# Optimization experiments

Measured on AMD Instinct MI355X. Metric: run time of the kernel, lower is better.

The kernel has to match this reference:

```python
import jax, jax.numpy as jnp
import numpy as np

N = 10000
E = 160000


def _lin(key, fi, fo):
    kw, kb = jax.random.split(key)
    W = jax.random.normal(kw, (fi, fo), dtype=jnp.float32) * 0.02
    b = jnp.zeros((fo,), dtype=jnp.float32)
    return W, b


def setup_inputs() -> dict:
    key = jax.random.key(0)
    ks = jax.random.split(key, 20)
    inp = {}
    inp['x'] = jax.random.normal(ks[0], (N, 2048), dtype=jnp.float32)
    src = jax.random.randint(ks[1], (E,), 0, N)
    dst = jax.random.randint(ks[2], (E,), 0, N)
    inp['edge_index'] = jnp.stack([src, dst]).astype(jnp.int64)
    dims = [(2048, 1024), (1024, 2048), (2048, 1024), (1024, 2048)]
    ki = 3
    for li, (fi, fo) in enumerate(dims, start=1):
        for name in ('q', 'k', 'v', 's'):
            W, b = _lin(ks[ki], fi, fo)
            ki += 1
            inp[f'W{li}{name}'] = W
            inp[f'b{li}{name}'] = b
    return inp


def _tconv(x, src, dst, Wq, bq, Wk, bk, Wv, bv, Ws, bs):
    # PyG TransformerConv, heads=1: per-edge attention j->i, softmax over
    # incoming edges of each target node i, plus root (skip) linear.
    q = x @ Wq + bq                      # [N, C]
    k = x @ Wk + bk
    v = x @ Wv + bv
    C = q.shape[-1]
    logits = jnp.sum(q[dst] * k[src], axis=-1) / jnp.sqrt(jnp.float32(C))  # [E]
    m = jax.ops.segment_max(logits, dst, num_segments=N)   # per-node max
    m = jnp.where(jnp.isfinite(m), m, 0.0)                  # isolated nodes
    e = jnp.exp(logits - m[dst])
    s = jax.ops.segment_sum(e, dst, num_segments=N)
    alpha = e / (s[dst] + 1e-16)                            # [E]
    agg = jax.ops.segment_sum(v[src] * alpha[:, None], dst, num_segments=N)
    return agg + x @ Ws + bs


def reference(x, edge_index,
              W1q, b1q, W1k, b1k, W1v, b1v, W1s, b1s,
              W2q, b2q, W2k, b2k, W2v, b2v, W2s, b2s,
              W3q, b3q, W3k, b3k, W3v, b3v, W3s, b3s,
              W4q, b4q, W4k, b4k, W4v, b4v, W4s, b4s):
    src, dst = edge_index[0], edge_index[1]
    h1 = jax.nn.elu(_tconv(x, src, dst, W1q, b1q, W1k, b1k, W1v, b1v, W1s, b1s))
    h2 = _tconv(h1, src, dst, W2q, b2q, W2k, b2k, W2v, b2v, W2s, b2s)
    h3 = jax.nn.elu(_tconv(h2, src, dst, W3q, b3q, W3k, b3k, W3v, b3v, W3s, b3s))
    out = _tconv(h3, src, dst, W4q, b4q, W4k, b4k, W4v, b4v, W4s, b4s)
    return out
```

## Files before the change

kernel.cpp:

```cpp
#include <hip/hip_runtime.h>
#include <cmath>
#include <cstddef>
#include <cstdint>

typedef __attribute__((ext_vector_type(8))) _Float16 half8_t;
typedef __attribute__((ext_vector_type(4))) _Float16 half4_t;
typedef __attribute__((ext_vector_type(2))) _Float16 half2_t;
typedef __attribute__((ext_vector_type(4))) float f32x4;

__device__ __forceinline__ float dot2f16(half2_t a, half2_t b, float c) {
#if __has_builtin(__builtin_amdgcn_fdot2)
  return __builtin_amdgcn_fdot2(a, b, c, false);
#else
  return c + (float)a.x * (float)b.x + (float)a.y * (float)b.y;
#endif
}

__device__ __forceinline__ void gload16(const unsigned short* g,
                                        unsigned short* l) {
  __builtin_amdgcn_global_load_lds(
      (const __attribute__((address_space(1))) unsigned int*)g,
      (__attribute__((address_space(3))) unsigned int*)l, 16, 0, 0);
}

__global__ __launch_bounds__(256) void cast_f16_k(
    const float* __restrict__ in, unsigned short* __restrict__ out, size_t n4) {
  size_t i = (size_t)blockIdx.x * blockDim.x + threadIdx.x;
  if (i >= n4) return;
  float4 v = ((const float4*)in)[i];
  half4_t h;
  h.x = (_Float16)v.x;
  h.y = (_Float16)v.y;
  h.z = (_Float16)v.z;
  h.w = (_Float16)v.w;
  ((half4_t*)out)[i] = h;
}

__global__ __launch_bounds__(256) void transp_f16_k(
    const float* __restrict__ W0, const float* __restrict__ W1,
    const float* __restrict__ W2, const float* __restrict__ W3,
    unsigned short* __restrict__ T, int K, int C) {
  __shared__ float t[32][33];
  const int m = blockIdx.z;
  const float* W = (m == 0) ? W0 : (m == 1) ? W1 : (m == 2) ? W2 : W3;
  _Float16* th = (_Float16*)T + (size_t)m * C * K;
  int k0 = blockIdx.x * 32, c0 = blockIdx.y * 32;
  int tx = threadIdx.x & 31, ty = threadIdx.x >> 5;
#pragma unroll
  for (int r = 0; r < 4; ++r)
    t[ty + r * 8][tx] = W[(size_t)(k0 + ty + r * 8) * C + c0 + tx];
  __syncthreads();
#pragma unroll
  for (int r = 0; r < 4; ++r) {
    int c = ty + r * 8;
    th[(size_t)(c0 + c) * K + k0 + tx] = (_Float16)t[tx][c];
  }
}

__global__ __launch_bounds__(512) void gemm_f16_k(
    const unsigned short* __restrict__ Ab, const unsigned short* __restrict__ Wt,
    const float* __restrict__ bq, const float* __restrict__ bk,
    const float* __restrict__ bv, const float* __restrict__ bs,
    unsigned short* __restrict__ Qh, unsigned short* __restrict__ Kh,
    unsigned short* __restrict__ Vh, float* __restrict__ S, int M, int K,
    int C, int NX, int NY) {
  __shared__ unsigned short lds[3][12288];

  const int nwg = NX * NY;
  const int bid = blockIdx.x;
  const int qq = nwg >> 3, rr = nwg & 7;
  const int xcd = bid & 7, idx = bid >> 3;
  const int wgid =
      (xcd < rr ? xcd * (qq + 1) : rr * (qq + 1) + (xcd - rr) * qq) + idx;
  const int by = wgid % NY, bx = wgid / NY;

  const int bm = bx * 256, n0 = by * 128;
  const int kind = n0 / C;
  const int tid = threadIdx.x;
  const int lane = tid & 63, w = tid >> 6;
  const int wm = w >> 1, wn = w & 1;
  const int fr = lane & 15, kg = lane >> 4;

  const int srow = w * 16 + (lane >> 2);
  const int soff = (((lane & 3) ^ ((lane >> 2) & 3))) * 8;
  const size_t ga0 = (size_t)min(bm + srow, M - 1) * K + soff;
  const size_t ga1 = (size_t)min(bm + srow + 128, M - 1) * K + soff;
  const size_t gb0 = (size_t)(n0 + srow) * K + soff;
  const int la0 = w * 512;
  const int la1 = 4096 + w * 512;
  const int lb0 = 8192 + w * 512;

  f32x4 acc[4][4];
#pragma unroll
  for (int i = 0; i < 4; ++i)
#pragma unroll
    for (int j = 0; j < 4; ++j) acc[i][j] = (f32x4)0.f;

  auto STAGE = [&](int buf, int ko) {
    gload16(Ab + ga0 + ko, &lds[buf][la0]);
    gload16(Ab + ga1 + ko, &lds[buf][la1]);
    gload16(Wt + gb0 + ko, &lds[buf][lb0]);
  };

  const int T = K / 32;
  STAGE(0, 0);
  STAGE(1, 32);

  const int rka = (kg ^ (fr & 3)) * 8;
  int buf = 0;
  for (int t = 0; t < T; ++t) {
    if (t + 1 < T)
      asm volatile("s_waitcnt vmcnt(3)" ::: "memory");
    else
      asm volatile("s_waitcnt vmcnt(0)" ::: "memory");
    __builtin_amdgcn_s_barrier();
    asm volatile("" ::: "memory");
    if (t + 2 < T) {
      int nb = buf + 2;
      if (nb >= 3) nb -= 3;
      STAGE(nb, (t + 2) * 32);
    }
    const unsigned short* As = lds[buf];
    const unsigned short* Bs = lds[buf] + 8192;
    half8_t ah[4], bh[4];
#pragma unroll
    for (int i = 0; i < 4; ++i) {
      ah[i] = *(const half8_t*)(As + (wm * 64 + i * 16 + fr) * 32 + rka);
      bh[i] = *(const half8_t*)(Bs + (wn * 64 + i * 16 + fr) * 32 + rka);
    }
#pragma unroll
    for (int i = 0; i < 4; ++i)
#pragma unroll
      for (int j = 0; j < 4; ++j)
        acc[i][j] = __builtin_amdgcn_mfma_f32_16x16x32_f16(ah[i], bh[j],
                                                           acc[i][j], 0, 0, 0);
    asm volatile("s_waitcnt lgkmcnt(0)" ::: "memory");
    buf = (buf == 2) ? 0 : buf + 1;
  }

  const float* bptr = (kind == 0) ? bq : (kind == 1) ? bk : (kind == 2) ? bv : bs;
  const int cbase = (n0 - kind * C) + wn * 64;
  float bvv[4];
#pragma unroll
  for (int j = 0; j < 4; ++j) bvv[j] = bptr[cbase + j * 16 + fr];

  unsigned short* obu = (kind == 0) ? Qh : (kind == 1) ? Kh : Vh;
  _Float16* ob = (_Float16*)obu;
#pragma unroll
  for (int i = 0; i < 4; ++i) {
#pragma unroll
    for (int r = 0; r < 4; ++r) {
      int gr = bm + wm * 64 + i * 16 + kg * 4 + r;
      if (gr < M) {
        if (kind == 3) {
#pragma unroll
          for (int j = 0; j < 4; ++j)
            S[(size_t)gr * C + cbase + j * 16 + fr] = acc[i][j][r] + bvv[j];
        } else {
#pragma unroll
          for (int j = 0; j < 4; ++j)
            ob[(size_t)gr * C + cbase + j * 16 + fr] =
                (_Float16)(acc[i][j][r] + bvv[j]);
        }
      }
    }
  }
}

__global__ __launch_bounds__(256) void attn_fused2_k(
    const unsigned short* __restrict__ Qh, const unsigned short* __restrict__ Kh,
    const unsigned short* __restrict__ Vh, const int* __restrict__ rowptr,
    const int* __restrict__ csr_src, float* __restrict__ gscratch,
    float* __restrict__ skipio, unsigned short* __restrict__ Hb, int C,
    float scale, int do_elu, int writeH) {
  __shared__ _Float16 qs[2048];
  __shared__ float ebuf[512];
  __shared__ int ssrc[512];
  __shared__ float wred[8];
  const int i = blockIdx.x;
  const int tid = threadIdx.x;
  const int lane = tid & 63, wid = tid >> 6;
  const int beg = rowptr[i], end = rowptr[i + 1];
  const int deg = end - beg;
  const bool sm = (deg <= 512);

  for (int c0 = tid * 4; c0 < C; c0 += 1024)
    *(uint2*)&qs[c0] = *(const uint2*)(Qh + (size_t)i * C + c0);
  if (sm)
    for (int p = tid; p < deg; p += 256) ssrc[p] = csr_src[beg + p];
  if (tid < 8) wred[tid] = (tid < 4) ? -INFINITY : 0.f;
  __syncthreads();

  if (deg > 0) {
    float wmaxv = -INFINITY;
    if (sm) {
      for (int ep = wid; ep < deg; ep += 8) {
        const int e1 = ep + 4;
        const bool h1 = e1 < deg;
        int s0 = ssrc[ep];
        int s1 = h1 ? ssrc[e1] : s0;
        const unsigned short* kr0 = Kh + (size_t)s0 * C;
        const unsigned short* kr1 = Kh + (size_t)s1 * C;
        float su0 = 0.f, su1 = 0.f;
        for (int c0 = lane * 8; c0 < C; c0 += 512) {
          uint4 k0 = *(const uint4*)(kr0 + c0);
          uint4 k1 = *(const uint4*)(kr1 + c0);
          uint4 qv = *(const uint4*)&qs[c0];
          const half2_t* kp0 = (const half2_t*)&k0;
          const half2_t* kp1 = (const half2_t*)&k1;
          const half2_t* qp = (const half2_t*)&qv;
#pragma unroll
          for (int u = 0; u < 4; ++u) {
            su0 = dot2f16(kp0[u], qp[u], su0);
            su1 = dot2f16(kp1[u], qp[u], su1);
          }
        }
#pragma unroll
        for (int o = 32; o; o >>= 1) {
          su0 += __shfl_xor(su0, o);
          su1 += __shfl_xor(su1, o);
        }
        float lg0 = su0 * scale;
        float lg1 = h1 ? su1 * scale : -INFINITY;
        if (lane == 0) {
          ebuf[ep] = lg0;
          if (h1) ebuf[e1] = lg1;
        }
        wmaxv = fmaxf(wmaxv, fmaxf(lg0, lg1));
      }
    } else {
      for (int ep = wid; ep < deg; ep += 4) {
        int s = csr_src[beg + ep];
        const unsigned short* kr = Kh + (size_t)s * C;
        float sum = 0.f;
        for (int c0 = lane * 8; c0 < C; c0 += 512) {
          uint4 kk = *(const uint4*)(kr + c0);
          uint4 qv = *(const uint4*)&qs[c0];
          const half2_t* kp = (const half2_t*)&kk;
          const half2_t* qp = (const half2_t*)&qv;
#pragma unroll
          for (int u = 0; u < 4; ++u) sum = dot2f16(kp[u], qp[u], sum);
        }
#pragma unroll
        for (int o = 32; o; o >>= 1) sum += __shfl_xor(sum, o);
        float lg = sum * scale;
        if (lane == 0) gscratch[beg + ep] = lg;
        wmaxv = fmaxf(wmaxv, lg);
      }
    }
    if (lane == 0) wred[wid] = wmaxv;
    __syncthreads();
    float m = fmaxf(fmaxf(wred[0], wred[1]), fmaxf(wred[2], wred[3]));

    float part = 0.f;
    for (int ep = tid; ep < deg; ep += 256) {
      float lg = sm ? ebuf[ep] : gscratch[beg + ep];
      float e = expf(lg - m);
      if (sm) ebuf[ep] = e; else gscratch[beg + ep] = e;
      part += e;
    }
#pragma unroll
    for (int o = 32; o; o >>= 1) part += __shfl_xor(part, o);
    if (lane == 0) wred[4 + wid] = part;
  }
  __syncthreads();

  float total = wred[4] + wred[5] + wred[6] + wred[7];
  float denom = 1.f / (total + 1e-16f);
  const int cpt = C >> 8;
  const int col0 = tid * cpt;
  float acc[8];
#pragma unroll
  for (int j = 0; j < 8; ++j) acc[j] = 0.f;

  if (sm) {
    int ep = 0;
    if (cpt == 8) {
      for (; ep + 4 <= deg; ep += 4) {
        float a0 = ebuf[ep] * denom, a1 = ebuf[ep + 1] * denom;
        float a2 = ebuf[ep + 2] * denom, a3 = ebuf[ep + 3] * denom;
        const unsigned short* v0 = Vh + (size_t)ssrc[ep] * C + col0;
        const unsigned short* v1 = Vh + (size_t)ssrc[ep + 1] * C + col0;
        const unsigned short* v2 = Vh + (size_t)ssrc[ep + 2] * C + col0;
        const unsigned short* v3 = Vh + (size_t)ssrc[ep + 3] * C + col0;
        uint4 p0 = *(const uint4*)v0, p1 = *(const uint4*)v1;
        uint4 p2 = *(const uint4*)v2, p3 = *(const uint4*)v3;
        const _Float16* h0 = (const _Float16*)&p0;
        const _Float16* h1 = (const _Float16*)&p1;
        const _Float16* h2 = (const _Float16*)&p2;
        const _Float16* h3 = (const _Float16*)&p3;
#pragma unroll
        for (int u = 0; u < 8; ++u) {
          acc[u] = fmaf(a0, (float)h0[u], acc[u]);
          acc[u] = fmaf(a1, (float)h1[u], acc[u]);
          acc[u] = fmaf(a2, (float)h2[u], acc[u]);
          acc[u] = fmaf(a3, (float)h3[u], acc[u]);
        }
      }
      for (; ep < deg; ++ep) {
        float a = ebuf[ep] * denom;
        uint4 pv = *(const uint4*)(Vh + (size_t)ssrc[ep] * C + col0);
        const _Float16* ph = (const _Float16*)&pv;
#pragma unroll
        for (int u = 0; u < 8; ++u) acc[u] = fmaf(a, (float)ph[u], acc[u]);
      }
    } else {
      for (; ep + 4 <= deg; ep += 4) {
        float a0 = ebuf[ep] * denom, a1 = ebuf[ep + 1] * denom;
        float a2 = ebuf[ep + 2] * denom, a3 = ebuf[ep + 3] * denom;
        ushort4 p0 = *(const ushort4*)(Vh + (size_t)ssrc[ep] * C + col0);
        ushort4 p1 = *(const ushort4*)(Vh + (size_t)ssrc[ep + 1] * C + col0);
        ushort4 p2 = *(const ushort4*)(Vh + (size_t)ssrc[ep + 2] * C + col0);
        ushort4 p3 = *(const ushort4*)(Vh + (size_t)ssrc[ep + 3] * C + col0);
        const _Float16* h0 = (const _Float16*)&p0;
        const _Float16* h1 = (const _Float16*)&p1;
        const _Float16* h2 = (const _Float16*)&p2;
        const _Float16* h3 = (const _Float16*)&p3;
#pragma unroll
        for (int u = 0; u < 4; ++u) {
          acc[u] = fmaf(a0, (float)h0[u], acc[u]);
          acc[u] = fmaf(a1, (float)h1[u], acc[u]);
          acc[u] = fmaf(a2, (float)h2[u], acc[u]);
          acc[u] = fmaf(a3, (float)h3[u], acc[u]);
        }
      }
      for (; ep < deg; ++ep) {
        float a = ebuf[ep] * denom;
        ushort4 pv = *(const ushort4*)(Vh + (size_t)ssrc[ep] * C + col0);
        const _Float16* ph = (const _Float16*)&pv;
#pragma unroll
        for (int u = 0; u < 4; ++u) acc[u] = fmaf(a, (float)ph[u], acc[u]);
      }
    }
  } else {
    for (int ep = 0; ep < deg; ++ep) {
      float a = gscratch[beg + ep] * denom;
      int s = csr_src[beg + ep];
      const unsigned short* vr = Vh + (size_t)s * C + col0;
      if (cpt == 4) {
        ushort4 pv = *(const ushort4*)vr;
        const _Float16* ph = (const _Float16*)&pv;
#pragma unroll
        for (int u = 0; u < 4; ++u) acc[u] = fmaf(a, (float)ph[u], acc[u]);
      } else {
        uint4 pv = *(const uint4*)vr;
        const _Float16* ph = (const _Float16*)&pv;
#pragma unroll
        for (int u = 0; u < 8; ++u) acc[u] = fmaf(a, (float)ph[u], acc[u]);
      }
    }
  }

  float* srow = skipio + (size_t)i * C + col0;
#pragma unroll
  for (int v4 = 0; v4 < 2; ++v4) {
    if (v4 * 4 < cpt) {
      float4 o = *(const float4*)(srow + v4 * 4);
      o.x += acc[v4 * 4 + 0];
      o.y += acc[v4 * 4 + 1];
      o.z += acc[v4 * 4 + 2];
      o.w += acc[v4 * 4 + 3];
      if (do_elu) {
        o.x = o.x > 0.f ? o.x : expm1f(o.x);
        o.y = o.y > 0.f ? o.y : expm1f(o.y);
        o.z = o.z > 0.f ? o.z : expm1f(o.z);
        o.w = o.w > 0.f ? o.w : expm1f(o.w);
      }
      if (writeH) {
        half4_t h;
        h.x = (_Float16)o.x;
        h.y = (_Float16)o.y;
        h.z = (_Float16)o.z;
        h.w = (_Float16)o.w;
        *(half4_t*)((_Float16*)Hb + (size_t)i * C + col0 + v4 * 4) = h;
      } else {
        *(float4*)(srow + v4 * 4) = o;
      }
    }
  }
}

__global__ void count_deg_k(const int* __restrict__ dst, int E,
                            int* __restrict__ cnt) {
  int e = blockIdx.x * blockDim.x + threadIdx.x;
  if (e < E) atomicAdd(&cnt[dst[e]], 1);
}

__global__ void scan_k(const int* __restrict__ cnt, int* __restrict__ rowptr,
                       int N) {
  __shared__ int part[1024];
  int t = threadIdx.x;
  int per = (N + 1023) >> 10;
  int base = t * per;
  int s = 0;
  for (int i = 0; i < per; ++i) {
    int idx = base + i;
    if (idx < N) s += cnt[idx];
  }
  part[t] = s;
  __syncthreads();
  for (int off = 1; off < 1024; off <<= 1) {
    int v = (t >= off) ? part[t - off] : 0;
    __syncthreads();
    part[t] += v;
    __syncthreads();
  }
  int run = part[t] - s;
  for (int i = 0; i < per; ++i) {
    int idx = base + i;
    if (idx < N) {
      rowptr[idx] = run;
      run += cnt[idx];
    }
  }
  if (t == 1023) rowptr[N] = part[1023];
}

__global__ void scatter_csr_k(const int* __restrict__ src,
                              const int* __restrict__ dst, int E,
                              const int* __restrict__ rowptr,
                              int* __restrict__ fill,
                              int* __restrict__ csr_src) {
  int e = blockIdx.x * blockDim.x + threadIdx.x;
  if (e >= E) return;
  int d = dst[e];
  int pos = rowptr[d] + atomicAdd(&fill[d], 1);
  csr_src[pos] = src[e];
}

extern "C" void kernel_launch(void* const* d_in, const int* in_sizes, int n_in,
                              void* d_out, int out_size, void* d_ws,
                              size_t ws_size, hipStream_t stream) {
  const float* x = (const float*)d_in[0];
  const int* eidx = (const int*)d_in[1];
  const int N = in_sizes[0] / 2048;
  const int E = in_sizes[1] / 2;
  const int* srcA = eidx;
  const int* dstA = eidx + E;
  float* dout = (float*)d_out;

  char* p = (char*)d_ws;
  auto alloc = [&](size_t bytes) {
    void* r = (void*)p;
    p += (bytes + 255) & ~(size_t)255;
    return r;
  };

  float* logits = (float*)alloc((size_t)E * 4);
  int* rowptr = (int*)alloc((size_t)(N + 1) * 4);
  int* cnt = (int*)alloc((size_t)N * 4);
  int* fill = (int*)alloc((size_t)N * 4);
  int* csr_src = (int*)alloc((size_t)E * 4);

  hipMemsetAsync(cnt, 0, (size_t)N * 4, stream);
  hipMemsetAsync(fill, 0, (size_t)N * 4, stream);
  count_deg_k<<<(E + 255) / 256, 256, 0, stream>>>(dstA, E, cnt);
  scan_k<<<1, 1024, 0, stream>>>(cnt, rowptr, N);
  scatter_csr_k<<<(E + 255) / 256, 256, 0, stream>>>(srcA, dstA, E, rowptr,
                                                     fill, csr_src);

  const size_t szH = (size_t)N * 2048 * 2;
  const size_t szWt = (size_t)4 * 1024 * 2048 * 2;

  unsigned short* Hb = (unsigned short*)alloc(szH);
  unsigned short* Qh = (unsigned short*)alloc(szH);
  unsigned short* Kh = (unsigned short*)alloc(szH);
  unsigned short* Vh = (unsigned short*)alloc(szH);
  unsigned short* Wt[4];
  for (int L = 0; L < 4; ++L) Wt[L] = (unsigned short*)alloc(szWt);

  const int fi[4] = {2048, 1024, 2048, 1024};
  const int fo[4] = {1024, 2048, 1024, 2048};
  const int elu[4] = {1, 0, 1, 0};

  cast_f16_k<<<(int)(((size_t)N * 2048 / 4 + 255) / 256), 256, 0, stream>>>(
      x, Hb, (size_t)N * 2048 / 4);

  for (int L = 0; L < 4; ++L) {
    const int K = fi[L], C = fo[L];
    const int b = 2 + L * 8;
    transp_f16_k<<<dim3(K / 32, C / 32, 4), 256, 0, stream>>>(
        (const float*)d_in[b + 0], (const float*)d_in[b + 2],
        (const float*)d_in[b + 4], (const float*)d_in[b + 6], Wt[L], K, C);
  }

  for (int L = 0; L < 4; ++L) {
    const int K = fi[L], C = fo[L];
    const int b = 2 + L * 8;
    const float scale = (float)(1.0 / sqrt((double)C));
    const int NX = (N + 255) / 256;
    const int NY = 4 * C / 128;
    gemm_f16_k<<<NX * NY, 512, 0, stream>>>(
        Hb, Wt[L], (const float*)d_in[b + 1], (const float*)d_in[b + 3],
        (const float*)d_in[b + 5], (const float*)d_in[b + 7], Qh, Kh, Vh, dout,
        N, K, C, NX, NY);
    attn_fused2_k<<<N, 256, 0, stream>>>(Qh, Kh, Vh, rowptr, csr_src, logits,
                                         dout, Hb, C, scale, elu[L],
                                         L < 3 ? 1 : 0);
  }
}
```

Before: 1.461 ms.

## Merge weight transposes, use online softmax, fp16 skip path, MFMA priority

Folds the four per-layer weight-transpose launches into a single 3D grid launch. In the attention kernel, the small-degree path now tracks a running max and sum per wave (online softmax), which removes the separate exponent pass and one barrier; the exponentials are recomputed in the aggregation loop instead. For layers 1-3 the skip-linear output is stored as fp16 in the output buffer to halve its write and read traffic, at some precision cost. It also raises wave priority around the MFMA block in the GEMM.

```diff
diff --git a/kernel.cpp b/kernel.cpp
--- a/kernel.cpp
+++ b/kernel.cpp
@@ -36,15 +36,21 @@
   ((half4_t*)out)[i] = h;
 }
 
-__global__ __launch_bounds__(256) void transp_f16_k(
-    const float* __restrict__ W0, const float* __restrict__ W1,
-    const float* __restrict__ W2, const float* __restrict__ W3,
-    unsigned short* __restrict__ T, int K, int C) {
+struct TranspAll {
+  const float* W[16];
+  unsigned short* T[4];
+};
+
+__global__ __launch_bounds__(256) void transp_all_k(TranspAll a) {
+  const int z = blockIdx.z;
+  const int L = z >> 2, m = z & 3;
+  const int K = (L & 1) ? 1024 : 2048;
+  const int C = (L & 1) ? 2048 : 1024;
+  const int k0 = blockIdx.x * 32, c0 = blockIdx.y * 32;
+  if (k0 >= K || c0 >= C) return;
   __shared__ float t[32][33];
-  const int m = blockIdx.z;
-  const float* W = (m == 0) ? W0 : (m == 1) ? W1 : (m == 2) ? W2 : W3;
-  _Float16* th = (_Float16*)T + (size_t)m * C * K;
-  int k0 = blockIdx.x * 32, c0 = blockIdx.y * 32;
+  const float* W = a.W[z];
+  _Float16* th = (_Float16*)a.T[L] + (size_t)m * C * K;
   int tx = threadIdx.x & 31, ty = threadIdx.x >> 5;
 #pragma unroll
   for (int r = 0; r < 4; ++r)
@@ -62,8 +68,9 @@
     const float* __restrict__ bq, const float* __restrict__ bk,
     const float* __restrict__ bv, const float* __restrict__ bs,
     unsigned short* __restrict__ Qh, unsigned short* __restrict__ Kh,
-    unsigned short* __restrict__ Vh, float* __restrict__ S, int M, int K,
-    int C, int NX, int NY) {
+    unsigned short* __restrict__ Vh, float* __restrict__ S,
+    unsigned short* __restrict__ Sh, int s16, int M, int K, int C, int NX,
+    int NY) {
   __shared__ unsigned short lds[3][12288];
 
   const int nwg = NX * NY;
@@ -128,12 +135,14 @@
       ah[i] = *(const half8_t*)(As + (wm * 64 + i * 16 + fr) * 32 + rka);
       bh[i] = *(const half8_t*)(Bs + (wn * 64 + i * 16 + fr) * 32 + rka);
     }
+    __builtin_amdgcn_s_setprio(1);
 #pragma unroll
     for (int i = 0; i < 4; ++i)
 #pragma unroll
       for (int j = 0; j < 4; ++j)
         acc[i][j] = __builtin_amdgcn_mfma_f32_16x16x32_f16(ah[i], bh[j],
                                                            acc[i][j], 0, 0, 0);
+    __builtin_amdgcn_s_setprio(0);
     asm volatile("s_waitcnt lgkmcnt(0)" ::: "memory");
     buf = (buf == 2) ? 0 : buf + 1;
   }
@@ -146,6 +155,7 @@
 
   unsigned short* obu = (kind == 0) ? Qh : (kind == 1) ? Kh : Vh;
   _Float16* ob = (_Float16*)obu;
+  _Float16* sh = (_Float16*)Sh;
 #pragma unroll
   for (int i = 0; i < 4; ++i) {
 #pragma unroll
@@ -153,9 +163,16 @@
       int gr = bm + wm * 64 + i * 16 + kg * 4 + r;
       if (gr < M) {
         if (kind == 3) {
-#pragma unroll
-          for (int j = 0; j < 4; ++j)
-            S[(size_t)gr * C + cbase + j * 16 + fr] = acc[i][j][r] + bvv[j];
+          if (s16) {
+#pragma unroll
+            for (int j = 0; j < 4; ++j)
+              sh[(size_t)gr * C + cbase + j * 16 + fr] =
+                  (_Float16)(acc[i][j][r] + bvv[j]);
+          } else {
+#pragma unroll
+            for (int j = 0; j < 4; ++j)
+              S[(size_t)gr * C + cbase + j * 16 + fr] = acc[i][j][r] + bvv[j];
+          }
         } else {
 #pragma unroll
           for (int j = 0; j < 4; ++j)
@@ -167,12 +184,13 @@
   }
 }
 
-__global__ __launch_bounds__(256) void attn_fused2_k(
+__global__ __launch_bounds__(256) void attn_fused3_k(
     const unsigned short* __restrict__ Qh, const unsigned short* __restrict__ Kh,
     const unsigned short* __restrict__ Vh, const int* __restrict__ rowptr,
     const int* __restrict__ csr_src, float* __restrict__ gscratch,
-    float* __restrict__ skipio, unsigned short* __restrict__ Hb, int C,
-    float scale, int do_elu, int writeH) {
+    float* __restrict__ skipio, const unsigned short* __restrict__ Sh16,
+    int skip16, unsigned short* __restrict__ Hb, int C, float scale,
+    int do_elu, int writeH) {
   __shared__ _Float16 qs[2048];
   __shared__ float ebuf[512];
   __shared__ int ssrc[512];
@@ -192,8 +210,8 @@
   __syncthreads();
 
   if (deg > 0) {
-    float wmaxv = -INFINITY;
     if (sm) {
+      float mw = -INFINITY, sw = 0.f;
       for (int ep = wid; ep < deg; ep += 8) {
         const int e1 = ep + 4;
         const bool h1 = e1 < deg;
@@ -226,9 +244,18 @@
           ebuf[ep] = lg0;
           if (h1) ebuf[e1] = lg1;
         }
-        wmaxv = fmaxf(wmaxv, fmaxf(lg0, lg1));
-      }
+        float nm = fmaxf(mw, fmaxf(lg0, lg1));
+        sw = sw * expf(mw - nm) + expf(lg0 - nm) +
+             (h1 ? expf(lg1 - nm) : 0.f);
+        mw = nm;
+      }
+      if (lane == 0) {
+        wred[wid] = mw;
+        wred[4 + wid] = sw;
+      }
+      __syncthreads();
     } else {
+      float wmaxv = -INFINITY;
       for (int ep = wid; ep < deg; ep += 4) {
         int s = csr_src[beg + ep];
         const unsigned short* kr = Kh + (size_t)s * C;
@@ -247,25 +274,32 @@
         if (lane == 0) gscratch[beg + ep] = lg;
         wmaxv = fmaxf(wmaxv, lg);
       }
-    }
-    if (lane == 0) wred[wid] = wmaxv;
+      if (lane == 0) wred[wid] = wmaxv;
+      __syncthreads();
+      float m = fmaxf(fmaxf(wred[0], wred[1]), fmaxf(wred[2], wred[3]));
+      float part = 0.f;
+      for (int ep = tid; ep < deg; ep += 256) {
+        float e = expf(gscratch[beg + ep] - m);
+        gscratch[beg + ep] = e;
+        part += e;
+      }
+#pragma unroll
+      for (int o = 32; o; o >>= 1) part += __shfl_xor(part, o);
+      if (lane == 0) wred[4 + wid] = part;
+      __syncthreads();
+    }
+  } else {
     __syncthreads();
-    float m = fmaxf(fmaxf(wred[0], wred[1]), fmaxf(wred[2], wred[3]));
-
-    float part = 0.f;
-    for (int ep = tid; ep < deg; ep += 256) {
-      float lg = sm ? ebuf[ep] : gscratch[beg + ep];
-      float e = expf(lg - m);
-      if (sm) ebuf[ep] = e; else gscratch[beg + ep] = e;
-      part += e;
-    }
-#pragma unroll
-    for (int o = 32; o; o >>= 1) part += __shfl_xor(part, o);
-    if (lane == 0) wred[4 + wid] = part;
-  }
-  __syncthreads();
-
-  float total = wred[4] + wred[5] + wred[6] + wred[7];
+  }
+
+  const float gmax = fmaxf(fmaxf(wred[0], wred[1]), fmaxf(wred[2], wred[3]));
+  float total;
+  if (sm) {
+    total = wred[4] * expf(wred[0] - gmax) + wred[5] * expf(wred[1] - gmax) +
+            wred[6] * expf(wred[2] - gmax) + wred[7] * expf(wred[3] - gmax);
+  } else {
+    total = wred[4] + wred[5] + wred[6] + wred[7];
+  }
   float denom = 1.f / (total + 1e-16f);
   const int cpt = C >> 8;
   const int col0 = tid * cpt;
@@ -277,14 +311,14 @@
     int ep = 0;
     if (cpt == 8) {
       for (; ep + 4 <= deg; ep += 4) {
-        float a0 = ebuf[ep] * denom, a1 = ebuf[ep + 1] * denom;
-        float a2 = ebuf[ep + 2] * denom, a3 = ebuf[ep + 3] * denom;
-        const unsigned short* v0 = Vh + (size_t)ssrc[ep] * C + col0;
-        const unsigned short* v1 = Vh + (size_t)ssrc[ep + 1] * C + col0;
-        const unsigned short* v2 = Vh + (size_t)ssrc[ep + 2] * C + col0;
-        const unsigned short* v3 = Vh + (size_t)ssrc[ep + 3] * C + col0;
-        uint4 p0 = *(const uint4*)v0, p1 = *(const uint4*)v1;
-        uint4 p2 = *(const uint4*)v2, p3 = *(const uint4*)v3;
+        float a0 = expf(ebuf[ep] - gmax) * denom;
+        float a1 = expf(ebuf[ep + 1] - gmax) * denom;
+        float a2 = expf(ebuf[ep + 2] - gmax) * denom;
+        float a3 = expf(ebuf[ep + 3] - gmax) * denom;
+        uint4 p0 = *(const uint4*)(Vh + (size_t)ssrc[ep] * C + col0);
+        uint4 p1 = *(const uint4*)(Vh + (size_t)ssrc[ep + 1] * C + col0);
+        uint4 p2 = *(const uint4*)(Vh + (size_t)ssrc[ep + 2] * C + col0);
+        uint4 p3 = *(const uint4*)(Vh + (size_t)ssrc[ep + 3] * C + col0);
         const _Float16* h0 = (const _Float16*)&p0;
         const _Float16* h1 = (const _Float16*)&p1;
         const _Float16* h2 = (const _Float16*)&p2;
@@ -298,7 +332,7 @@
         }
       }
       for (; ep < deg; ++ep) {
-        float a = ebuf[ep] * denom;
+        float a = expf(ebuf[ep] - gmax) * denom;
         uint4 pv = *(const uint4*)(Vh + (size_t)ssrc[ep] * C + col0);
         const _Float16* ph = (const _Float16*)&pv;
 #pragma unroll
@@ -306,8 +340,10 @@
       }
     } else {
       for (; ep + 4 <= deg; ep += 4) {
-        float a0 = ebuf[ep] * denom, a1 = ebuf[ep + 1] * denom;
-        float a2 = ebuf[ep + 2] * denom, a3 = ebuf[ep + 3] * denom;
+        float a0 = expf(ebuf[ep] - gmax) * denom;
+        float a1 = expf(ebuf[ep + 1] - gmax) * denom;
+        float a2 = expf(ebuf[ep + 2] - gmax) * denom;
+        float a3 = expf(ebuf[ep + 3] - gmax) * denom;
         ushort4 p0 = *(const ushort4*)(Vh + (size_t)ssrc[ep] * C + col0);
         ushort4 p1 = *(const ushort4*)(Vh + (size_t)ssrc[ep + 1] * C + col0);
         ushort4 p2 = *(const ushort4*)(Vh + (size_t)ssrc[ep + 2] * C + col0);
@@ -325,7 +361,7 @@
         }
       }
       for (; ep < deg; ++ep) {
-        float a = ebuf[ep] * denom;
+        float a = expf(ebuf[ep] - gmax) * denom;
         ushort4 pv = *(const ushort4*)(Vh + (size_t)ssrc[ep] * C + col0);
         const _Float16* ph = (const _Float16*)&pv;
 #pragma unroll
@@ -355,7 +391,14 @@
 #pragma unroll
   for (int v4 = 0; v4 < 2; ++v4) {
     if (v4 * 4 < cpt) {
-      float4 o = *(const float4*)(srow + v4 * 4);
+      float4 o;
+      if (skip16) {
+        ushort4 s4 = *(const ushort4*)(Sh16 + (size_t)i * C + col0 + v4 * 4);
+        const _Float16* sp = (const _Float16*)&s4;
+        o = make_float4((float)sp[0], (float)sp[1], (float)sp[2], (float)sp[3]);
+      } else {
+        o = *(const float4*)(srow + v4 * 4);
+      }
       o.x += acc[v4 * 4 + 0];
       o.y += acc[v4 * 4 + 1];
       o.z += acc[v4 * 4 + 2];
@@ -476,13 +519,15 @@
   cast_f16_k<<<(int)(((size_t)N * 2048 / 4 + 255) / 256), 256, 0, stream>>>(
       x, Hb, (size_t)N * 2048 / 4);
 
+  TranspAll ta;
   for (int L = 0; L < 4; ++L) {
-    const int K = fi[L], C = fo[L];
-    const int b = 2 + L * 8;
-    transp_f16_k<<<dim3(K / 32, C / 32, 4), 256, 0, stream>>>(
-        (const float*)d_in[b + 0], (const float*)d_in[b + 2],
-        (const float*)d_in[b + 4], (const float*)d_in[b + 6], Wt[L], K, C);
-  }
+    for (int m = 0; m < 4; ++m)
+      ta.W[L * 4 + m] = (const float*)d_in[2 + L * 8 + 2 * m];
+    ta.T[L] = Wt[L];
+  }
+  transp_all_k<<<dim3(64, 64, 16), 256, 0, stream>>>(ta);
+
+  unsigned short* Sh = (unsigned short*)dout;
 
   for (int L = 0; L < 4; ++L) {
     const int K = fi[L], C = fo[L];
@@ -490,12 +535,13 @@
     const float scale = (float)(1.0 / sqrt((double)C));
     const int NX = (N + 255) / 256;
     const int NY = 4 * C / 128;
+    const int s16 = (L < 3) ? 1 : 0;
     gemm_f16_k<<<NX * NY, 512, 0, stream>>>(
         Hb, Wt[L], (const float*)d_in[b + 1], (const float*)d_in[b + 3],
         (const float*)d_in[b + 5], (const float*)d_in[b + 7], Qh, Kh, Vh, dout,
-        N, K, C, NX, NY);
-    attn_fused2_k<<<N, 256, 0, stream>>>(Qh, Kh, Vh, rowptr, csr_src, logits,
-                                         dout, Hb, C, scale, elu[L],
+        Sh, s16, N, K, C, NX, NY);
+    attn_fused3_k<<<N, 256, 0, stream>>>(Qh, Kh, Vh, rowptr, csr_src, logits,
+                                         dout, Sh, s16, Hb, C, scale, elu[L],
                                          L < 3 ? 1 : 0);
   }
 }
```

Measured after the change: 1.449 ms. About the same (-0.8%).
